# Performance work log

Measured on AMD Instinct MI355X. Metric: run time of the kernel, lower is better.

The kernel has to match this reference:

```python
import jax, jax.numpy as jnp
import numpy as np

B, F_IN, D_IN = 1024, 64, 64
N_CAPS, D_CAPS = 32, 64
ROUTINGS = 3
HEADS = 2
EPS = 1e-7  # K.epsilon()


def setup_inputs() -> dict:
    key = jax.random.key(0)
    ks = jax.random.split(key, 8)
    P = N_CAPS * (N_CAPS - 1) // 2
    return {
        "x": jax.random.normal(ks[0], (B, F_IN, D_IN), jnp.float32),
        "reweight_W": jax.random.normal(ks[1], (D_IN, N_CAPS, D_CAPS), jnp.float32) * 0.05,
        "routing_init": 10.0 * jax.random.truncated_normal(ks[2], -2.0, 2.0, (N_CAPS, F_IN), jnp.float32),
        "kernel_fm": jnp.full((N_CAPS, 1), 0.5, jnp.float32),
        "bias_fm": jnp.zeros((D_CAPS,), jnp.float32),
        "kernel_mf": jnp.ones((P, 1), jnp.float32),
        "bias_mf": jnp.zeros((D_CAPS,), jnp.float32),
        "kernel_highint": jnp.full((N_CAPS, 1), 0.5, jnp.float32),
        "bias_highint": jnp.zeros((D_CAPS * HEADS,), jnp.float32),
        "W_query": jax.random.normal(ks[3], (D_CAPS, D_CAPS * HEADS), jnp.float32) * 0.05,
        "W_key": jax.random.normal(ks[4], (D_CAPS, D_CAPS * HEADS), jnp.float32) * 0.05,
        "W_value": jax.random.normal(ks[5], (D_CAPS, D_CAPS * HEADS), jnp.float32) * 0.05,
        "W_res": jax.random.normal(ks[6], (D_CAPS, D_CAPS * HEADS), jnp.float32) * 0.05,
    }


def _squash(v):
    s = jnp.sum(v * v, axis=-1, keepdims=True) + EPS
    return (jnp.sqrt(s) / (0.5 + s)) * v


def _heads(t):
    # [B,N,H*F] -> [H,B,N,F] (matches tf.stack(tf.split(t, H, axis=2)))
    b, n, _ = t.shape
    return t.reshape(b, n, HEADS, D_CAPS).transpose(2, 0, 1, 3)


def reference(x, reweight_W, routing_init, kernel_fm, bias_fm, kernel_mf, bias_mf,
              kernel_highint, bias_highint, W_query, W_key, W_value, W_res):
    # inputs_hat: [B, N, F, C]
    inputs_hat = jnp.einsum('bfd,dnc->bnfc', x, reweight_W)
    b_logits = jnp.broadcast_to(routing_init[None], (x.shape[0], N_CAPS, F_IN))
    for _ in range(ROUTINGS):
        c = jax.nn.softmax(b_logits, axis=1)            # softmax over capsules
        outputs = _squash(jnp.einsum('bnf,bnfc->bnc', c, inputs_hat))
        b_logits = b_logits + jnp.einsum('bnc,bnfc->bnf', outputs, inputs_hat)
    c = jax.nn.softmax(b_logits, axis=1)
    routing_score = c[..., None]                        # [B,N,F,1]
    attention_output = routing_score * inputs_hat       # [B,N,F,C]

    # FM per-field: square-of-sum minus sum-of-square over input capsules
    sum_f = jnp.sum(attention_output, axis=2)           # [B,N,C]
    field_fm = sum_f ** 2 - jnp.sum(attention_output ** 2, axis=2)
    hi_fm = jnp.sum(field_fm * kernel_fm[None], axis=1) + bias_fm  # [B,C]

    field_wise_vectors = sum_f                          # [B,N,C]

    # pairwise MF interactions (itertools.combinations order == triu indices)
    li, ri = np.triu_indices(N_CAPS, k=1)
    emb_prod = field_wise_vectors[:, li] * field_wise_vectors[:, ri]  # [B,P,C]
    h_mf = jnp.sum(emb_prod * kernel_mf[None], axis=1) + bias_mf      # [B,C]

    # InteractingLayer (multi-head self-attention over fields, use_res=True)
    q = _heads(jnp.einsum('bnd,de->bne', field_wise_vectors, W_query))  # [H,B,N,F]
    k = _heads(jnp.einsum('bnd,de->bne', field_wise_vectors, W_key))
    v = _heads(jnp.einsum('bnd,de->bne', field_wise_vectors, W_value))
    attn = jax.nn.softmax(jnp.einsum('hbnf,hbmf->hbnm', q, k), axis=-1)
    out = jnp.einsum('hbnm,hbmf->hbnf', attn, v)        # [H,B,N,F]
    out = out.transpose(1, 2, 0, 3).reshape(x.shape[0], N_CAPS, HEADS * D_CAPS)
    res = jnp.einsum('bnd,de->bne', field_wise_vectors, W_res)
    fv2 = jax.nn.relu(out + res)                        # [B,N,H*F]
    high_int = jnp.sum(fv2 * kernel_highint[None], axis=1) + bias_highint  # [B,2C]

    return jnp.concatenate([hi_fm, h_mf, high_int], axis=-1), routing_score
```

## Files before the change

### kernel.cpp

```cpp
#include <hip/hip_runtime.h>


#define EPS_SQ 1e-7f

typedef __attribute__((ext_vector_type(8))) short bf16x8;
typedef __attribute__((ext_vector_type(4))) float floatx4;

__device__ __forceinline__ int lidx(int r, int c) {
  return r * 68 + ((((c >> 2) ^ (r >> 2)) & 15) << 2) + (c & 3);
}
__device__ __forceinline__ unsigned short f2bf(float f) {
  unsigned u = __float_as_uint(f);
  u += 0x7FFFu + ((u >> 16) & 1u);
  return (unsigned short)(u >> 16);
}

__global__ __launch_bounds__(256) void k_upd(
    const float* __restrict__ x, const float* __restrict__ rinit,
    const float* __restrict__ ow, float* __restrict__ blog,
    float* __restrict__ xc, float* __restrict__ rs, int iter)
{
  __shared__ __align__(16) float xs[64 * 68];
  __shared__ __align__(16) float owS[32 * 68];
  __shared__ __align__(16) float bS[32 * 68];
  const int b = blockIdx.x, t = threadIdx.x;
  const float* xb = x + b * 4096;

#pragma unroll
  for (int k = 0; k < 4; k++) {
    int lin = t + 256 * k; int f = lin >> 4; int d0 = (lin & 15) << 2;
    *(float4*)&xs[lidx(f, d0)] = *(const float4*)(xb + f * 64 + d0);
  }
  {
    const float* src = (iter <= 1) ? rinit : (blog + b * 2048);
#pragma unroll
    for (int k = 0; k < 2; k++) {
      int lin = t + 256 * k; int n = lin >> 4; int f0 = (lin & 15) << 2;
      *(float4*)&bS[lidx(n, f0)] = *(const float4*)(src + n * 64 + f0);
    }
  }
  if (iter > 0) {
#pragma unroll
    for (int k = 0; k < 2; k++) {
      int lin = t + 256 * k; int n = lin >> 4; int d0 = (lin & 15) << 2;
      *(float4*)&owS[lidx(n, d0)] = *(const float4*)(ow + b * 2048 + n * 64 + d0);
    }
  }
  __syncthreads();

  const int tn = t >> 4, tlo = t & 15;

  if (iter > 0) {
    const int n0 = tn * 2, f0 = tlo * 4;
    float acc[2][4] = {{0, 0, 0, 0}, {0, 0, 0, 0}};
    for (int dq = 0; dq < 64; dq += 4) {
      float o[2][4];
      *(float4*)o[0] = *(const float4*)&owS[lidx(n0, dq)];
      *(float4*)o[1] = *(const float4*)&owS[lidx(n0 + 1, dq)];
#pragma unroll
      for (int i = 0; i < 4; i++) {
        float xr[4];
        *(float4*)xr = *(const float4*)&xs[lidx(f0 + i, dq)];
#pragma unroll
        for (int k = 0; k < 4; k++) {
          acc[0][i] += o[0][k] * xr[k];
          acc[1][i] += o[1][k] * xr[k];
        }
      }
    }
#pragma unroll
    for (int j = 0; j < 2; j++) {
      float tmp[4];
      *(float4*)tmp = *(const float4*)&bS[lidx(n0 + j, f0)];
#pragma unroll
      for (int i = 0; i < 4; i++) tmp[i] += acc[j][i];
      *(float4*)&bS[lidx(n0 + j, f0)] = *(float4*)tmp;
    }
    __syncthreads();
    if (iter < 3) {
#pragma unroll
      for (int k = 0; k < 2; k++) {
        int lin = t + 256 * k; int n = lin >> 4; int f0b = (lin & 15) << 2;
        *(float4*)(blog + b * 2048 + n * 64 + f0b) = *(const float4*)&bS[lidx(n, f0b)];
      }
    }
    __syncthreads();
  }

  {
    const int n = t & 31, fg = t >> 5;
#pragma unroll
    for (int k = 0; k < 8; k++) {
      int f = fg * 8 + k;
      float v = bS[lidx(n, f)];
      float m = v;
      for (int s = 16; s > 0; s >>= 1) m = fmaxf(m, __shfl_xor(m, s, 64));
      float e = __expf(v - m);
      float sum = e;
      for (int s = 16; s > 0; s >>= 1) sum += __shfl_xor(sum, s, 64);
      bS[lidx(n, f)] = e / sum;
    }
  }
  __syncthreads();

  if (iter == 3) {
#pragma unroll
    for (int k = 0; k < 8; k++) {
      int lin = t + 256 * k; int n = lin >> 6, f = lin & 63;
      rs[b * 2048 + n * 64 + f] = bS[lidx(n, f)];
    }
  }
  {
    const int n0 = tn * 2, d0 = tlo * 4;
    float acc[2][4] = {{0, 0, 0, 0}, {0, 0, 0, 0}};
    for (int f = 0; f < 64; f++) {
      float c0v = bS[lidx(n0, f)];
      float c1v = bS[lidx(n0 + 1, f)];
      float xr[4];
      *(float4*)xr = *(const float4*)&xs[lidx(f, d0)];
#pragma unroll
      for (int i = 0; i < 4; i++) {
        acc[0][i] += c0v * xr[i];
        acc[1][i] += c1v * xr[i];
      }
    }
#pragma unroll
    for (int j = 0; j < 2; j++)
      *(float4*)(xc + b * 2048 + (n0 + j) * 64 + d0) = *(float4*)acc[j];
  }
}

__global__ __launch_bounds__(256) void k_prepq(
    const float* __restrict__ W, float* __restrict__ Qb)
{
  __shared__ __align__(16) float Mn[64 * 68];
  const int n = blockIdx.x, t = threadIdx.x;
#pragma unroll
  for (int k = 0; k < 4; k++) {
    int lin = t + 256 * k; int d = lin >> 4; int c0 = (lin & 15) << 2;
    *(float4*)&Mn[lidx(d, c0)] = *(const float4*)(W + d * 2048 + n * 64 + c0);
  }
  __syncthreads();
  const int d1 = (t >> 4) * 4, d2 = (t & 15) * 4;
  float acc[4][4] = {};
  for (int cq = 0; cq < 64; cq += 4) {
    float m1[4][4], m2[4][4];
#pragma unroll
    for (int i = 0; i < 4; i++) *(float4*)m1[i] = *(const float4*)&Mn[lidx(d1 + i, cq)];
#pragma unroll
    for (int j = 0; j < 4; j++) *(float4*)m2[j] = *(const float4*)&Mn[lidx(d2 + j, cq)];
#pragma unroll
    for (int i = 0; i < 4; i++)
#pragma unroll
      for (int j = 0; j < 4; j++) {
        float s = 0.f;
#pragma unroll
        for (int k = 0; k < 4; k++) s += m1[i][k] * m2[j][k];
        acc[i][j] += s;
      }
  }
#pragma unroll
  for (int i = 0; i < 4; i++)
    *(float4*)(Qb + n * 4096 + (d1 + i) * 64 + d2) = *(float4*)acc[i];
}

__global__ __launch_bounds__(256) void k_sowq(
    const float* __restrict__ Qb, const float* __restrict__ xc,
    float* __restrict__ ow)
{
  __shared__ __align__(16) float Qs[64 * 68];
  __shared__ __align__(16) float xcS[32 * 68];
  const int n = blockIdx.x & 31, b0 = (blockIdx.x >> 5) * 32, t = threadIdx.x;

#pragma unroll
  for (int k = 0; k < 4; k++) {
    int lin = t + 256 * k; int d1 = lin >> 4; int d2 = (lin & 15) << 2;
    *(float4*)&Qs[lidx(d1, d2)] = *(const float4*)(Qb + n * 4096 + d1 * 64 + d2);
  }
#pragma unroll
  for (int k = 0; k < 2; k++) {
    int lin = t + 256 * k; int bb = lin >> 4; int d0 = (lin & 15) << 2;
    *(float4*)&xcS[lidx(bb, d0)] = *(const float4*)(xc + (b0 + bb) * 2048 + n * 64 + d0);
  }
  __syncthreads();

  const int bb0 = (t >> 4) * 2, d4 = (t & 15) * 4;
  float y0[4] = {}, y1[4] = {};
  for (int dq = 0; dq < 64; dq += 4) {
    float x0[4], x1[4];
    *(float4*)x0 = *(const float4*)&xcS[lidx(bb0, dq)];
    *(float4*)x1 = *(const float4*)&xcS[lidx(bb0 + 1, dq)];
#pragma unroll
    for (int j = 0; j < 4; j++) {
      float qr[4];
      *(float4*)qr = *(const float4*)&Qs[lidx(dq + j, d4)];
#pragma unroll
      for (int c = 0; c < 4; c++) {
        y0[c] += x0[j] * qr[c];
        y1[c] += x1[j] * qr[c];
      }
    }
  }
  float xa[4], xb2[4];
  *(float4*)xa = *(const float4*)&xcS[lidx(bb0, d4)];
  *(float4*)xb2 = *(const float4*)&xcS[lidx(bb0 + 1, d4)];
  float s0 = 0.f, s1 = 0.f;
#pragma unroll
  for (int c = 0; c < 4; c++) { s0 += y0[c] * xa[c]; s1 += y1[c] * xb2[c]; }
#pragma unroll
  for (int sh = 1; sh <= 8; sh <<= 1) {
    s0 += __shfl_xor(s0, sh, 64);
    s1 += __shfl_xor(s1, sh, 64);
  }
  s0 += EPS_SQ; s1 += EPS_SQ;
  const float sc0 = sqrtf(s0) / (0.5f + s0);
  const float sc1 = sqrtf(s1) / (0.5f + s1);
  float o0[4], o1[4];
#pragma unroll
  for (int c = 0; c < 4; c++) { o0[c] = y0[c] * sc0; o1[c] = y1[c] * sc1; }
  *(float4*)(ow + (b0 + bb0) * 2048 + n * 64 + d4) = *(float4*)o0;
  *(float4*)(ow + (b0 + bb0 + 1) * 2048 + n * 64 + d4) = *(float4*)o1;
}

__global__ __launch_bounds__(256) void k_fwv(
    const float* __restrict__ W, const float* __restrict__ xc,
    float* __restrict__ fwv)
{
  __shared__ __align__(16) float Mn[64 * 68];
  __shared__ __align__(16) float xcS[32 * 68];
  const int n = blockIdx.x & 31, b0 = (blockIdx.x >> 5) * 32, t = threadIdx.x;

#pragma unroll
  for (int k = 0; k < 4; k++) {
    int lin = t + 256 * k; int d = lin >> 4; int c0 = (lin & 15) << 2;
    *(float4*)&Mn[lidx(d, c0)] = *(const float4*)(W + d * 2048 + n * 64 + c0);
  }
#pragma unroll
  for (int k = 0; k < 2; k++) {
    int lin = t + 256 * k; int bb = lin >> 4; int d0 = (lin & 15) << 2;
    *(float4*)&xcS[lidx(bb, d0)] = *(const float4*)(xc + (b0 + bb) * 2048 + n * 64 + d0);
  }
  __syncthreads();

  const int bb0 = (t >> 4) * 2, c4 = (t & 15) * 4;
  float acc[2][4] = {};
  for (int dq = 0; dq < 64; dq += 4) {
    float xv0[4], xv1[4];
    *(float4*)xv0 = *(const float4*)&xcS[lidx(bb0, dq)];
    *(float4*)xv1 = *(const float4*)&xcS[lidx(bb0 + 1, dq)];
#pragma unroll
    for (int j = 0; j < 4; j++) {
      float mr[4];
      *(float4*)mr = *(const float4*)&Mn[lidx(dq + j, c4)];
#pragma unroll
      for (int c = 0; c < 4; c++) {
        acc[0][c] += xv0[j] * mr[c];
        acc[1][c] += xv1[j] * mr[c];
      }
    }
  }
  *(float4*)(fwv + (b0 + bb0) * 2048 + n * 64 + c4) = *(float4*)acc[0];
  *(float4*)(fwv + (b0 + bb0 + 1) * 2048 + n * 64 + c4) = *(float4*)acc[1];
}

__global__ __launch_bounds__(256) void k_ih(
    const float* __restrict__ x, const float* __restrict__ W,
    const float* __restrict__ rs, float* __restrict__ ssq)
{
  __shared__ __align__(16) unsigned short xB[4 * 64 * 64];
  __shared__ __align__(16) unsigned short wB[2 * 64 * 64];
  __shared__ unsigned short cF2[4 * 8 * 64];
  const int n_oct = (blockIdx.x & 3) << 3, b0 = (blockIdx.x >> 2) * 4;
  const int t = threadIdx.x, w = t >> 6, lane = t & 63;

#pragma unroll
  for (int k = 0; k < 16; k++) {
    int ch = t + 256 * k;
    int bb = ch >> 10, rem = ch & 1023;
    int f = rem >> 4, fq = rem & 15;
    int dg = fq >> 1, half = fq & 1;
    float4 v = *(const float4*)(x + ((b0 + bb) * 64 + f) * 64 + fq * 4);
    unsigned p0 = f2bf(v.x) | ((unsigned)f2bf(v.y) << 16);
    unsigned p1 = f2bf(v.z) | ((unsigned)f2bf(v.w) << 16);
    *(uint2*)&xB[bb * 4096 + f * 64 + ((dg ^ (f & 7)) << 3) + half * 4] =
        make_uint2(p0, p1);
  }
#pragma unroll
  for (int nn = 0; nn < 8; nn++) {
    float v = rs[(b0 + w) * 2048 + (n_oct + nn) * 64 + lane];
    cF2[(w * 8 + nn) * 64 + lane] = f2bf(v * v);
  }
  __syncthreads();

  const int m = lane & 15, q = lane >> 4, ms = m & 7;
  bf16x8 a[4][2];
#pragma unroll
  for (int mi = 0; mi < 4; mi++) {
    const unsigned short* bp = xB + w * 4096 + (mi * 16 + m) * 64;
#pragma unroll
    for (int kk = 0; kk < 2; kk++)
      a[mi][kk] = *(const bf16x8*)&bp[((kk * 4 + q) ^ ms) << 3];
  }

  for (int np = 0; np < 4; np++) {
    const int n0 = n_oct + np * 2;
    __syncthreads();
    {
      int dd = t >> 2, cq = t & 3;
      int dg = dd >> 3, dl = dd & 7;
#pragma unroll
      for (int nn = 0; nn < 2; nn++) {
        const float* wp = W + dd * 2048 + (n0 + nn) * 64 + cq * 16;
        unsigned short* base = wB + nn * 4096;
#pragma unroll
        for (int i4 = 0; i4 < 4; i4++) {
          float4 v = *(const float4*)(wp + i4 * 4);
          float vv[4] = {v.x, v.y, v.z, v.w};
#pragma unroll
          for (int j = 0; j < 4; j++) {
            int c = cq * 16 + i4 * 4 + j;
            base[c * 64 + ((dg ^ (c & 7)) << 3) + dl] = f2bf(vv[j]);
          }
        }
      }
    }
    __syncthreads();
#pragma unroll
    for (int nn = 0; nn < 2; nn++) {
      bf16x8 bf[4][2];
#pragma unroll
      for (int ci = 0; ci < 4; ci++) {
        const unsigned short* bp = wB + nn * 4096 + (ci * 16 + m) * 64;
#pragma unroll
        for (int kk = 0; kk < 2; kk++)
          bf[ci][kk] = *(const bf16x8*)&bp[((kk * 4 + q) ^ ms) << 3];
      }
      float ps[4] = {0.f, 0.f, 0.f, 0.f};
      const unsigned short* cf = cF2 + (w * 8 + np * 2 + nn) * 64 + q * 4;
#pragma unroll
      for (int mi = 0; mi < 4; mi++) {
        float cfv[4];
#pragma unroll
        for (int r = 0; r < 4; r++)
          cfv[r] = __uint_as_float((unsigned)cf[mi * 16 + r] << 16);
#pragma unroll
        for (int ci = 0; ci < 4; ci++) {
          floatx4 c0 = {0.f, 0.f, 0.f, 0.f};
          c0 = __builtin_amdgcn_mfma_f32_16x16x32_bf16(a[mi][0], bf[ci][0], c0, 0, 0, 0);
          c0 = __builtin_amdgcn_mfma_f32_16x16x32_bf16(a[mi][1], bf[ci][1], c0, 0, 0, 0);
#pragma unroll
          for (int r = 0; r < 4; r++) { float tv = c0[r]; ps[ci] += cfv[r] * tv * tv; }
        }
      }
#pragma unroll
      for (int ci = 0; ci < 4; ci++) {
        ps[ci] += __shfl_xor(ps[ci], 16, 64);
        ps[ci] += __shfl_xor(ps[ci], 32, 64);
      }
      if (q == 0) {
#pragma unroll
        for (int ci = 0; ci < 4; ci++)
          ssq[(b0 + w) * 2048 + (n0 + nn) * 64 + ci * 16 + m] = ps[ci];
      }
    }
  }
}

__global__ __launch_bounds__(256) void k_prep(
    const float* __restrict__ Wq, const float* __restrict__ Wk,
    const float* __restrict__ kmf, float* __restrict__ Ab, float* __restrict__ Kb)
{
  const int t = threadIdx.x;
  if (blockIdx.x < 8) {
    __shared__ __align__(16) float wkS[64 * 68];
    __shared__ __align__(16) float wqS[16 * 68];
    const int h = blockIdx.x & 1, rg = blockIdx.x >> 1;
#pragma unroll
    for (int k = 0; k < 4; k++) {
      int lin = t + 256 * k; int dp = lin >> 4; int e0 = (lin & 15) << 2;
      *(float4*)&wkS[lidx(dp, e0)] = *(const float4*)(Wk + dp * 128 + h * 64 + e0);
    }
    {
      int dl = t >> 4, e0 = (t & 15) << 2;
      *(float4*)&wqS[lidx(dl, e0)] = *(const float4*)(Wq + (rg * 16 + dl) * 128 + h * 64 + e0);
    }
    __syncthreads();
    const int dl = t >> 4, dp0 = (t & 15) << 2;
    float acc[4] = {};
    for (int e = 0; e < 64; e += 4) {
      float q4[4];
      *(float4*)q4 = *(const float4*)&wqS[lidx(dl, e)];
#pragma unroll
      for (int c = 0; c < 4; c++) {
        float mr[4];
        *(float4*)mr = *(const float4*)&wkS[lidx(dp0 + c, e)];
        acc[c] += q4[0] * mr[0] + q4[1] * mr[1] + q4[2] * mr[2] + q4[3] * mr[3];
      }
    }
    *(float4*)(Ab + h * 4096 + (rg * 16 + dl) * 64 + dp0) = *(float4*)acc;
  } else {
    __shared__ float Ks[1024];
    *(float4*)&Ks[t * 4] = make_float4(0.f, 0.f, 0.f, 0.f);
    __syncthreads();
    if (t < 248) {
#pragma unroll
      for (int j = 0; j < 2; j++) {
        int p = t * 2 + j;
        if (p < 496) {
          int l = 0, rem = p;
          while (rem >= 31 - l) { rem -= 31 - l; ++l; }
          int r = l + 1 + rem;
          float v = kmf[p];
          Ks[l * 32 + r] = v;
          Ks[r * 32 + l] = v;
        }
      }
    }
    __syncthreads();
    *(float4*)&Kb[t * 4] = *(const float4*)&Ks[t * 4];
  }
}

__global__ __launch_bounds__(256) void k_attn(
    const float* __restrict__ fwv, const float* __restrict__ ssq,
    const float* __restrict__ Ab, const float* __restrict__ Kb,
    const float* __restrict__ Wv, const float* __restrict__ Wr,
    const float* __restrict__ kfm, const float* __restrict__ bfm,
    const float* __restrict__ bmf, const float* __restrict__ khi,
    const float* __restrict__ bhi, float* __restrict__ out0)
{
  __shared__ __align__(16) float smem[8832];
  float* fwS  = smem;
  float* pS   = smem + 2176;
  float* bufA = smem + 4480;
  float* tS   = smem + 6656;
  float* vS   = smem + 4480;
  float* redH = smem + 2176;
  float* Kf   = smem + 4480;
  float* red1 = smem + 5504;

  const int b = blockIdx.x, t = threadIdx.x;
  const int tn = t >> 4, te = t & 15;
  const int n0 = tn * 2, e0 = te * 8, d0 = te * 4;

#pragma unroll
  for (int k = 0; k < 2; k++) {
    int lin = t + 256 * k; int nn = lin >> 4; int c0 = (lin & 15) << 2;
    *(float4*)&fwS[lidx(nn, c0)] = *(const float4*)(fwv + b * 2048 + nn * 64 + c0);
  }
  __syncthreads();

  for (int h = 0; h < 2; h++) {
    float tacc[2][4] = {};
    for (int half = 0; half < 2; half++) {
#pragma unroll
      for (int k = 0; k < 2; k++) {
        int lin = t + 256 * k; int d = lin >> 4; int c0 = (lin & 15) << 2;
        *(float4*)&bufA[lidx(d, c0)] =
            *(const float4*)(Ab + h * 4096 + (half * 32 + d) * 64 + c0);
      }
      __syncthreads();
      for (int dq = 0; dq < 32; dq += 4) {
        float fw0[4], fw1[4];
        *(float4*)fw0 = *(const float4*)&fwS[lidx(n0, half * 32 + dq)];
        *(float4*)fw1 = *(const float4*)&fwS[lidx(n0 + 1, half * 32 + dq)];
#pragma unroll
        for (int j = 0; j < 4; j++) {
          float mr[4];
          *(float4*)mr = *(const float4*)&bufA[lidx(dq + j, d0)];
#pragma unroll
          for (int c = 0; c < 4; c++) {
            tacc[0][c] += fw0[j] * mr[c];
            tacc[1][c] += fw1[j] * mr[c];
          }
        }
      }
      __syncthreads();
    }
    *(float4*)&tS[lidx(n0, d0)] = *(float4*)tacc[0];
    *(float4*)&tS[lidx(n0 + 1, d0)] = *(float4*)tacc[1];
    __syncthreads();
    {
      const int m0 = te * 2;
      float s00 = 0.f, s01 = 0.f, s10 = 0.f, s11 = 0.f;
      for (int kk = 0; kk < 16; kk++) {
        float ta0[4], ta1[4], f0[4], f1[4];
        *(float4*)ta0 = *(const float4*)&tS[lidx(n0, kk * 4)];
        *(float4*)ta1 = *(const float4*)&tS[lidx(n0 + 1, kk * 4)];
        *(float4*)f0 = *(const float4*)&fwS[lidx(m0, kk * 4)];
        *(float4*)f1 = *(const float4*)&fwS[lidx(m0 + 1, kk * 4)];
#pragma unroll
        for (int j = 0; j < 4; j++) {
          s00 += ta0[j] * f0[j]; s01 += ta0[j] * f1[j];
          s10 += ta1[j] * f0[j]; s11 += ta1[j] * f1[j];
        }
      }
      pS[(h * 32 + n0) * 36 + m0] = s00;
      pS[(h * 32 + n0) * 36 + m0 + 1] = s01;
      pS[(h * 32 + n0 + 1) * 36 + m0] = s10;
      pS[(h * 32 + n0 + 1) * 36 + m0 + 1] = s11;
    }
    __syncthreads();
  }

  {
    const int r = t >> 2, sub = t & 3;
    const int base = r * 36 + sub * 8;
    float v0[4], v1[4];
    *(float4*)v0 = *(const float4*)&pS[base];
    *(float4*)v1 = *(const float4*)&pS[base + 4];
    float mx = fmaxf(fmaxf(fmaxf(v0[0], v0[1]), fmaxf(v0[2], v0[3])),
                     fmaxf(fmaxf(v1[0], v1[1]), fmaxf(v1[2], v1[3])));
    mx = fmaxf(mx, __shfl_xor(mx, 1, 64));
    mx = fmaxf(mx, __shfl_xor(mx, 2, 64));
    float sum = 0.f;
#pragma unroll
    for (int j = 0; j < 4; j++) { v0[j] = __expf(v0[j] - mx); sum += v0[j]; }
#pragma unroll
    for (int j = 0; j < 4; j++) { v1[j] = __expf(v1[j] - mx); sum += v1[j]; }
    sum += __shfl_xor(sum, 1, 64);
    sum += __shfl_xor(sum, 2, 64);
    const float inv = 1.0f / sum;
#pragma unroll
    for (int j = 0; j < 4; j++) { v0[j] *= inv; v1[j] *= inv; }
    *(float4*)&pS[base] = *(float4*)v0;
    *(float4*)&pS[base + 4] = *(float4*)v1;
  }
  __syncthreads();

  {
    float acc[2][8] = {};
    for (int dq = 0; dq < 64; dq += 4) {
      float fw0[4], fw1[4];
      *(float4*)fw0 = *(const float4*)&fwS[lidx(n0, dq)];
      *(float4*)fw1 = *(const float4*)&fwS[lidx(n0 + 1, dq)];
#pragma unroll
      for (int jj = 0; jj < 4; jj++) {
        float w8[8];
        *(float4*)&w8[0] = *(const float4*)(Wv + (dq + jj) * 128 + e0);
        *(float4*)&w8[4] = *(const float4*)(Wv + (dq + jj) * 128 + e0 + 4);
#pragma unroll
        for (int j = 0; j < 8; j++) {
          acc[0][j] += fw0[jj] * w8[j];
          acc[1][j] += fw1[jj] * w8[j];
        }
      }
    }
    *(float4*)&vS[n0 * 132 + e0] = *(float4*)&acc[0][0];
    *(float4*)&vS[n0 * 132 + e0 + 4] = *(float4*)&acc[0][4];
    *(float4*)&vS[(n0 + 1) * 132 + e0] = *(float4*)&acc[1][0];
    *(float4*)&vS[(n0 + 1) * 132 + e0 + 4] = *(float4*)&acc[1][4];
  }
  __syncthreads();

  {
    const int h2 = te >> 3;
    float pacc[2][8] = {};
    for (int m = 0; m < 32; m++) {
      float p0 = pS[(h2 * 32 + n0) * 36 + m];
      float p1 = pS[(h2 * 32 + n0 + 1) * 36 + m];
      float vr[8];
      *(float4*)&vr[0] = *(const float4*)&vS[m * 132 + e0];
      *(float4*)&vr[4] = *(const float4*)&vS[m * 132 + e0 + 4];
#pragma unroll
      for (int j = 0; j < 8; j++) {
        pacc[0][j] += p0 * vr[j];
        pacc[1][j] += p1 * vr[j];
      }
    }
    for (int dq = 0; dq < 64; dq += 4) {
      float fw0[4], fw1[4];
      *(float4*)fw0 = *(const float4*)&fwS[lidx(n0, dq)];
      *(float4*)fw1 = *(const float4*)&fwS[lidx(n0 + 1, dq)];
#pragma unroll
      for (int jj = 0; jj < 4; jj++) {
        float w8[8];
        *(float4*)&w8[0] = *(const float4*)(Wr + (dq + jj) * 128 + e0);
        *(float4*)&w8[4] = *(const float4*)(Wr + (dq + jj) * 128 + e0 + 4);
#pragma unroll
        for (int j = 0; j < 8; j++) {
          pacc[0][j] += fw0[jj] * w8[j];
          pacc[1][j] += fw1[jj] * w8[j];
        }
      }
    }
    __syncthreads();
    {
      float kh0 = khi[n0], kh1 = khi[n0 + 1];
      float ph[8];
#pragma unroll
      for (int j = 0; j < 8; j++)
        ph[j] = kh0 * fmaxf(pacc[0][j], 0.f) + kh1 * fmaxf(pacc[1][j], 0.f);
      *(float4*)&redH[tn * 132 + e0] = *(float4*)&ph[0];
      *(float4*)&redH[tn * 132 + e0 + 4] = *(float4*)&ph[4];
    }
  }
  *(float4*)&Kf[t * 4] = *(const float4*)(Kb + t * 4);
  __syncthreads();

  if (t < 128) {
    float s = 0.f;
#pragma unroll
    for (int k = 0; k < 16; k++) s += redH[k * 132 + t];
    out0[b * 256 + 128 + t] = s + bhi[t];
  }
  {
    const int c = t & 63, nq = t >> 6;
    float p = 0.f;
#pragma unroll
    for (int k = 0; k < 8; k++) {
      int nn = nq * 8 + k;
      float fv = fwS[lidx(nn, c)];
      float sv = ssq[b * 2048 + nn * 64 + c];
      p += (fv * fv - sv) * kfm[nn];
    }
    red1[nq * 68 + c] = p;
    float inner[8] = {};
    for (int r = 0; r < 32; r++) {
      float fr = fwS[lidx(r, c)];
#pragma unroll
      for (int l8 = 0; l8 < 8; l8++)
        inner[l8] += Kf[(nq * 8 + l8) * 32 + r] * fr;
    }
    float hmf = 0.f;
#pragma unroll
    for (int l8 = 0; l8 < 8; l8++)
      hmf += fwS[lidx(nq * 8 + l8, c)] * inner[l8];
    red1[(4 + nq) * 68 + c] = hmf;
  }
  __syncthreads();
  if (t < 64) {
    out0[b * 256 + t] = red1[t] + red1[68 + t] + red1[136 + t] + red1[204 + t] + bfm[t];
    float h2 = red1[272 + t] + red1[340 + t] + red1[408 + t] + red1[476 + t];
    out0[b * 256 + 64 + t] = 0.5f * h2 + bmf[t];
  }
}

extern "C" void kernel_launch(void* const* d_in, const int* in_sizes, int n_in,
                              void* d_out, int out_size, void* d_ws, size_t ws_size,
                              hipStream_t stream) {
  (void)in_sizes; (void)n_in; (void)out_size; (void)ws_size;
  const float* x     = (const float*)d_in[0];
  const float* W     = (const float*)d_in[1];
  const float* rinit = (const float*)d_in[2];
  const float* kfm   = (const float*)d_in[3];
  const float* bfm   = (const float*)d_in[4];
  const float* kmf   = (const float*)d_in[5];
  const float* bmf   = (const float*)d_in[6];
  const float* khi   = (const float*)d_in[7];
  const float* bhi   = (const float*)d_in[8];
  const float* Wq    = (const float*)d_in[9];
  const float* Wk    = (const float*)d_in[10];
  const float* Wv    = (const float*)d_in[11];
  const float* Wr    = (const float*)d_in[12];

  float* out0 = (float*)d_out;
  float* rs   = out0 + 1024 * 256;
  float* Qbuf = rs;

  float* ws   = (float*)d_ws;
  float* xc   = ws;
  float* ow   = ws + 2097152;
  float* blog = ws + 2 * 2097152;
  float* fwv  = ow;
  float* ssq  = blog;
  float* Abuf = xc;
  float* Kbuf = xc + 8192;

  k_prepq<<<32, 256, 0, stream>>>(W, Qbuf);
  k_upd<<<1024, 256, 0, stream>>>(x, rinit, ow, blog, xc, rs, 0);
  for (int it = 1; it <= 3; it++) {
    k_sowq<<<1024, 256, 0, stream>>>(Qbuf, xc, ow);
    k_upd<<<1024, 256, 0, stream>>>(x, rinit, ow, blog, xc, rs, it);
  }
  k_fwv<<<1024, 256, 0, stream>>>(W, xc, fwv);
  k_prep<<<9, 256, 0, stream>>>(Wq, Wk, kmf, Abuf, Kbuf);
  k_ih<<<1024, 256, 0, stream>>>(x, W, rs, ssq);
  k_attn<<<1024, 256, 0, stream>>>(fwv, ssq, Abuf, Kbuf, Wv, Wr,
                                   kfm, bfm, bmf, khi, bhi, out0);
}
```

Measured before the change: 280.5 us.

## Fuse all routing iterations and field-wise projection into one per-batch kernel

Replaces the alternating k_upd/k_sowq launches (seven kernels) and k_fwv with a single k_route2 kernel. Each block keeps one batch's logits, coupling coefficients, xc and outputs in shared memory across all routing iterations. The Q-matrix and W reads now come straight from global memory (via cache) instead of being staged per block. The three prep kernels merge into one 41-block launch. This removes launch overhead and the global round-trips of xc, ow and blog, at the cost of more shared memory per block and uncoalesced-ish per-thread reads of Q and W.

```diff
diff --git a/kernel.cpp b/kernel.cpp
--- a/kernel.cpp
+++ b/kernel.cpp
@@ -15,252 +15,236 @@
   return (unsigned short)(u >> 16);
 }
 
-__global__ __launch_bounds__(256) void k_upd(
-    const float* __restrict__ x, const float* __restrict__ rinit,
-    const float* __restrict__ ow, float* __restrict__ blog,
-    float* __restrict__ xc, float* __restrict__ rs, int iter)
+__global__ __launch_bounds__(256) void k_prep2(
+    const float* __restrict__ W, const float* __restrict__ Wq,
+    const float* __restrict__ Wk, const float* __restrict__ kmf,
+    float* __restrict__ Qb, float* __restrict__ Ab, float* __restrict__ Kb)
+{
+  const int t = threadIdx.x;
+  if (blockIdx.x < 32) {
+    __shared__ __align__(16) float Mn[64 * 68];
+    const int n = blockIdx.x;
+#pragma unroll
+    for (int k = 0; k < 4; k++) {
+      int lin = t + 256 * k; int d = lin >> 4; int c0 = (lin & 15) << 2;
+      *(float4*)&Mn[lidx(d, c0)] = *(const float4*)(W + d * 2048 + n * 64 + c0);
+    }
+    __syncthreads();
+    const int d1 = (t >> 4) * 4, d2 = (t & 15) * 4;
+    float acc[4][4] = {};
+    for (int cq = 0; cq < 64; cq += 4) {
+      float m1[4][4], m2[4][4];
+#pragma unroll
+      for (int i = 0; i < 4; i++) *(float4*)m1[i] = *(const float4*)&Mn[lidx(d1 + i, cq)];
+#pragma unroll
+      for (int j = 0; j < 4; j++) *(float4*)m2[j] = *(const float4*)&Mn[lidx(d2 + j, cq)];
+#pragma unroll
+      for (int i = 0; i < 4; i++)
+#pragma unroll
+        for (int j = 0; j < 4; j++) {
+          float s = 0.f;
+#pragma unroll
+          for (int k = 0; k < 4; k++) s += m1[i][k] * m2[j][k];
+          acc[i][j] += s;
+        }
+    }
+#pragma unroll
+    for (int i = 0; i < 4; i++)
+      *(float4*)(Qb + n * 4096 + (d1 + i) * 64 + d2) = *(float4*)acc[i];
+  } else if (blockIdx.x < 40) {
+    __shared__ __align__(16) float wkS[64 * 68];
+    __shared__ __align__(16) float wqS[16 * 68];
+    const int hb = blockIdx.x - 32;
+    const int h = hb & 1, rg = hb >> 1;
+#pragma unroll
+    for (int k = 0; k < 4; k++) {
+      int lin = t + 256 * k; int dp = lin >> 4; int e0 = (lin & 15) << 2;
+      *(float4*)&wkS[lidx(dp, e0)] = *(const float4*)(Wk + dp * 128 + h * 64 + e0);
+    }
+    {
+      int dl = t >> 4, e0 = (t & 15) << 2;
+      *(float4*)&wqS[lidx(dl, e0)] = *(const float4*)(Wq + (rg * 16 + dl) * 128 + h * 64 + e0);
+    }
+    __syncthreads();
+    const int dl = t >> 4, dp0 = (t & 15) << 2;
+    float acc[4] = {};
+    for (int e = 0; e < 64; e += 4) {
+      float q4[4];
+      *(float4*)q4 = *(const float4*)&wqS[lidx(dl, e)];
+#pragma unroll
+      for (int c = 0; c < 4; c++) {
+        float mr[4];
+        *(float4*)mr = *(const float4*)&wkS[lidx(dp0 + c, e)];
+        acc[c] += q4[0] * mr[0] + q4[1] * mr[1] + q4[2] * mr[2] + q4[3] * mr[3];
+      }
+    }
+    *(float4*)(Ab + h * 4096 + (rg * 16 + dl) * 64 + dp0) = *(float4*)acc;
+  } else {
+    __shared__ float Ks[1024];
+    *(float4*)&Ks[t * 4] = make_float4(0.f, 0.f, 0.f, 0.f);
+    __syncthreads();
+    if (t < 248) {
+#pragma unroll
+      for (int j = 0; j < 2; j++) {
+        int p = t * 2 + j;
+        if (p < 496) {
+          int l = 0, rem = p;
+          while (rem >= 31 - l) { rem -= 31 - l; ++l; }
+          int r = l + 1 + rem;
+          float v = kmf[p];
+          Ks[l * 32 + r] = v;
+          Ks[r * 32 + l] = v;
+        }
+      }
+    }
+    __syncthreads();
+    *(float4*)&Kb[t * 4] = *(const float4*)&Ks[t * 4];
+  }
+}
+
+__global__ __launch_bounds__(256) void k_route2(
+    const float* __restrict__ x, const float* __restrict__ W,
+    const float* __restrict__ rinit, const float* __restrict__ Qb,
+    float* __restrict__ rs, float* __restrict__ fwv)
 {
   __shared__ __align__(16) float xs[64 * 68];
+  __shared__ __align__(16) float bS[32 * 68];
+  __shared__ __align__(16) float cS[32 * 68];
+  __shared__ __align__(16) float xcS[32 * 68];
   __shared__ __align__(16) float owS[32 * 68];
-  __shared__ __align__(16) float bS[32 * 68];
   const int b = blockIdx.x, t = threadIdx.x;
-  const float* xb = x + b * 4096;
+  const int tn = t >> 4, tlo = t & 15;
+  const int nq = t >> 3, sub = t & 7;
 
 #pragma unroll
   for (int k = 0; k < 4; k++) {
     int lin = t + 256 * k; int f = lin >> 4; int d0 = (lin & 15) << 2;
-    *(float4*)&xs[lidx(f, d0)] = *(const float4*)(xb + f * 64 + d0);
-  }
+    *(float4*)&xs[lidx(f, d0)] = *(const float4*)(x + b * 4096 + f * 64 + d0);
+  }
+#pragma unroll
+  for (int k = 0; k < 2; k++) {
+    int lin = t + 256 * k; int n = lin >> 4; int f0 = (lin & 15) << 2;
+    *(float4*)&bS[lidx(n, f0)] = *(const float4*)(rinit + n * 64 + f0);
+  }
+  __syncthreads();
+
+  for (int it = 0; it < 4; it++) {
+    {
+      const int nl = t & 31, fg = t >> 5;
+#pragma unroll
+      for (int k = 0; k < 8; k++) {
+        int f = fg * 8 + k;
+        float v = bS[lidx(nl, f)];
+        float m = v;
+        for (int s = 16; s > 0; s >>= 1) m = fmaxf(m, __shfl_xor(m, s, 64));
+        float e = __expf(v - m);
+        float sum = e;
+        for (int s = 16; s > 0; s >>= 1) sum += __shfl_xor(sum, s, 64);
+        cS[lidx(nl, f)] = e / sum;
+      }
+    }
+    __syncthreads();
+    if (it == 3) {
+#pragma unroll
+      for (int k = 0; k < 8; k++) {
+        int lin = t + 256 * k; int n = lin >> 6, f = lin & 63;
+        rs[b * 2048 + n * 64 + f] = cS[lidx(n, f)];
+      }
+    }
+    {
+      const int n0 = tn * 2, d0 = tlo * 4;
+      float acc[2][4] = {{0, 0, 0, 0}, {0, 0, 0, 0}};
+      for (int f = 0; f < 64; f++) {
+        float c0v = cS[lidx(n0, f)];
+        float c1v = cS[lidx(n0 + 1, f)];
+        float xr[4];
+        *(float4*)xr = *(const float4*)&xs[lidx(f, d0)];
+#pragma unroll
+        for (int i = 0; i < 4; i++) {
+          acc[0][i] += c0v * xr[i];
+          acc[1][i] += c1v * xr[i];
+        }
+      }
+      *(float4*)&xcS[lidx(n0, d0)] = *(float4*)acc[0];
+      *(float4*)&xcS[lidx(n0 + 1, d0)] = *(float4*)acc[1];
+    }
+    __syncthreads();
+    if (it == 3) break;
+
+    {
+      const float* Qn = Qb + nq * 4096 + sub * 8;
+      float y[8] = {};
+#pragma unroll 4
+      for (int d1 = 0; d1 < 64; d1++) {
+        float xv = xcS[lidx(nq, d1)];
+        float4 qa = *(const float4*)(Qn + d1 * 64);
+        float4 qb2 = *(const float4*)(Qn + d1 * 64 + 4);
+        y[0] += xv * qa.x; y[1] += xv * qa.y; y[2] += xv * qa.z; y[3] += xv * qa.w;
+        y[4] += xv * qb2.x; y[5] += xv * qb2.y; y[6] += xv * qb2.z; y[7] += xv * qb2.w;
+      }
+      float xa[4], xb2[4];
+      *(float4*)xa = *(const float4*)&xcS[lidx(nq, sub * 8)];
+      *(float4*)xb2 = *(const float4*)&xcS[lidx(nq, sub * 8 + 4)];
+      float ps = y[0] * xa[0] + y[1] * xa[1] + y[2] * xa[2] + y[3] * xa[3]
+               + y[4] * xb2[0] + y[5] * xb2[1] + y[6] * xb2[2] + y[7] * xb2[3];
+      ps += __shfl_xor(ps, 1, 64);
+      ps += __shfl_xor(ps, 2, 64);
+      ps += __shfl_xor(ps, 4, 64);
+      const float ss = ps + EPS_SQ;
+      const float sc = sqrtf(ss) / (0.5f + ss);
+      float o0[4] = {y[0] * sc, y[1] * sc, y[2] * sc, y[3] * sc};
+      float o1[4] = {y[4] * sc, y[5] * sc, y[6] * sc, y[7] * sc};
+      *(float4*)&owS[lidx(nq, sub * 8)] = *(float4*)o0;
+      *(float4*)&owS[lidx(nq, sub * 8 + 4)] = *(float4*)o1;
+    }
+    __syncthreads();
+
+    {
+      const int n0 = tn * 2, f0 = tlo * 4;
+      float acc[2][4] = {{0, 0, 0, 0}, {0, 0, 0, 0}};
+      for (int dq = 0; dq < 64; dq += 4) {
+        float o[2][4];
+        *(float4*)o[0] = *(const float4*)&owS[lidx(n0, dq)];
+        *(float4*)o[1] = *(const float4*)&owS[lidx(n0 + 1, dq)];
+#pragma unroll
+        for (int i = 0; i < 4; i++) {
+          float xr[4];
+          *(float4*)xr = *(const float4*)&xs[lidx(f0 + i, dq)];
+#pragma unroll
+          for (int k = 0; k < 4; k++) {
+            acc[0][i] += o[0][k] * xr[k];
+            acc[1][i] += o[1][k] * xr[k];
+          }
+        }
+      }
+#pragma unroll
+      for (int j = 0; j < 2; j++) {
+        float tmp[4];
+        *(float4*)tmp = *(const float4*)&bS[lidx(n0 + j, f0)];
+#pragma unroll
+        for (int i = 0; i < 4; i++) tmp[i] += acc[j][i];
+        *(float4*)&bS[lidx(n0 + j, f0)] = *(float4*)tmp;
+      }
+    }
+    __syncthreads();
+  }
+
   {
-    const float* src = (iter <= 1) ? rinit : (blog + b * 2048);
-#pragma unroll
-    for (int k = 0; k < 2; k++) {
-      int lin = t + 256 * k; int n = lin >> 4; int f0 = (lin & 15) << 2;
-      *(float4*)&bS[lidx(n, f0)] = *(const float4*)(src + n * 64 + f0);
-    }
-  }
-  if (iter > 0) {
-#pragma unroll
-    for (int k = 0; k < 2; k++) {
-      int lin = t + 256 * k; int n = lin >> 4; int d0 = (lin & 15) << 2;
-      *(float4*)&owS[lidx(n, d0)] = *(const float4*)(ow + b * 2048 + n * 64 + d0);
-    }
-  }
-  __syncthreads();
-
-  const int tn = t >> 4, tlo = t & 15;
-
-  if (iter > 0) {
-    const int n0 = tn * 2, f0 = tlo * 4;
-    float acc[2][4] = {{0, 0, 0, 0}, {0, 0, 0, 0}};
-    for (int dq = 0; dq < 64; dq += 4) {
-      float o[2][4];
-      *(float4*)o[0] = *(const float4*)&owS[lidx(n0, dq)];
-      *(float4*)o[1] = *(const float4*)&owS[lidx(n0 + 1, dq)];
-#pragma unroll
-      for (int i = 0; i < 4; i++) {
-        float xr[4];
-        *(float4*)xr = *(const float4*)&xs[lidx(f0 + i, dq)];
-#pragma unroll
-        for (int k = 0; k < 4; k++) {
-          acc[0][i] += o[0][k] * xr[k];
-          acc[1][i] += o[1][k] * xr[k];
-        }
-      }
-    }
-#pragma unroll
-    for (int j = 0; j < 2; j++) {
-      float tmp[4];
-      *(float4*)tmp = *(const float4*)&bS[lidx(n0 + j, f0)];
-#pragma unroll
-      for (int i = 0; i < 4; i++) tmp[i] += acc[j][i];
-      *(float4*)&bS[lidx(n0 + j, f0)] = *(float4*)tmp;
-    }
-    __syncthreads();
-    if (iter < 3) {
-#pragma unroll
-      for (int k = 0; k < 2; k++) {
-        int lin = t + 256 * k; int n = lin >> 4; int f0b = (lin & 15) << 2;
-        *(float4*)(blog + b * 2048 + n * 64 + f0b) = *(const float4*)&bS[lidx(n, f0b)];
-      }
-    }
-    __syncthreads();
-  }
-
-  {
-    const int n = t & 31, fg = t >> 5;
-#pragma unroll
-    for (int k = 0; k < 8; k++) {
-      int f = fg * 8 + k;
-      float v = bS[lidx(n, f)];
-      float m = v;
-      for (int s = 16; s > 0; s >>= 1) m = fmaxf(m, __shfl_xor(m, s, 64));
-      float e = __expf(v - m);
-      float sum = e;
-      for (int s = 16; s > 0; s >>= 1) sum += __shfl_xor(sum, s, 64);
-      bS[lidx(n, f)] = e / sum;
-    }
-  }
-  __syncthreads();
-
-  if (iter == 3) {
-#pragma unroll
-    for (int k = 0; k < 8; k++) {
-      int lin = t + 256 * k; int n = lin >> 6, f = lin & 63;
-      rs[b * 2048 + n * 64 + f] = bS[lidx(n, f)];
-    }
-  }
-  {
-    const int n0 = tn * 2, d0 = tlo * 4;
-    float acc[2][4] = {{0, 0, 0, 0}, {0, 0, 0, 0}};
-    for (int f = 0; f < 64; f++) {
-      float c0v = bS[lidx(n0, f)];
-      float c1v = bS[lidx(n0 + 1, f)];
-      float xr[4];
-      *(float4*)xr = *(const float4*)&xs[lidx(f, d0)];
-#pragma unroll
-      for (int i = 0; i < 4; i++) {
-        acc[0][i] += c0v * xr[i];
-        acc[1][i] += c1v * xr[i];
-      }
-    }
-#pragma unroll
-    for (int j = 0; j < 2; j++)
-      *(float4*)(xc + b * 2048 + (n0 + j) * 64 + d0) = *(float4*)acc[j];
-  }
-}
-
-__global__ __launch_bounds__(256) void k_prepq(
-    const float* __restrict__ W, float* __restrict__ Qb)
-{
-  __shared__ __align__(16) float Mn[64 * 68];
-  const int n = blockIdx.x, t = threadIdx.x;
-#pragma unroll
-  for (int k = 0; k < 4; k++) {
-    int lin = t + 256 * k; int d = lin >> 4; int c0 = (lin & 15) << 2;
-    *(float4*)&Mn[lidx(d, c0)] = *(const float4*)(W + d * 2048 + n * 64 + c0);
-  }
-  __syncthreads();
-  const int d1 = (t >> 4) * 4, d2 = (t & 15) * 4;
-  float acc[4][4] = {};
-  for (int cq = 0; cq < 64; cq += 4) {
-    float m1[4][4], m2[4][4];
-#pragma unroll
-    for (int i = 0; i < 4; i++) *(float4*)m1[i] = *(const float4*)&Mn[lidx(d1 + i, cq)];
-#pragma unroll
-    for (int j = 0; j < 4; j++) *(float4*)m2[j] = *(const float4*)&Mn[lidx(d2 + j, cq)];
-#pragma unroll
-    for (int i = 0; i < 4; i++)
-#pragma unroll
-      for (int j = 0; j < 4; j++) {
-        float s = 0.f;
-#pragma unroll
-        for (int k = 0; k < 4; k++) s += m1[i][k] * m2[j][k];
-        acc[i][j] += s;
-      }
-  }
-#pragma unroll
-  for (int i = 0; i < 4; i++)
-    *(float4*)(Qb + n * 4096 + (d1 + i) * 64 + d2) = *(float4*)acc[i];
-}
-
-__global__ __launch_bounds__(256) void k_sowq(
-    const float* __restrict__ Qb, const float* __restrict__ xc,
-    float* __restrict__ ow)
-{
-  __shared__ __align__(16) float Qs[64 * 68];
-  __shared__ __align__(16) float xcS[32 * 68];
-  const int n = blockIdx.x & 31, b0 = (blockIdx.x >> 5) * 32, t = threadIdx.x;
-
-#pragma unroll
-  for (int k = 0; k < 4; k++) {
-    int lin = t + 256 * k; int d1 = lin >> 4; int d2 = (lin & 15) << 2;
-    *(float4*)&Qs[lidx(d1, d2)] = *(const float4*)(Qb + n * 4096 + d1 * 64 + d2);
-  }
-#pragma unroll
-  for (int k = 0; k < 2; k++) {
-    int lin = t + 256 * k; int bb = lin >> 4; int d0 = (lin & 15) << 2;
-    *(float4*)&xcS[lidx(bb, d0)] = *(const float4*)(xc + (b0 + bb) * 2048 + n * 64 + d0);
-  }
-  __syncthreads();
-
-  const int bb0 = (t >> 4) * 2, d4 = (t & 15) * 4;
-  float y0[4] = {}, y1[4] = {};
-  for (int dq = 0; dq < 64; dq += 4) {
-    float x0[4], x1[4];
-    *(float4*)x0 = *(const float4*)&xcS[lidx(bb0, dq)];
-    *(float4*)x1 = *(const float4*)&xcS[lidx(bb0 + 1, dq)];
-#pragma unroll
-    for (int j = 0; j < 4; j++) {
-      float qr[4];
-      *(float4*)qr = *(const float4*)&Qs[lidx(dq + j, d4)];
-#pragma unroll
-      for (int c = 0; c < 4; c++) {
-        y0[c] += x0[j] * qr[c];
-        y1[c] += x1[j] * qr[c];
-      }
-    }
-  }
-  float xa[4], xb2[4];
-  *(float4*)xa = *(const float4*)&xcS[lidx(bb0, d4)];
-  *(float4*)xb2 = *(const float4*)&xcS[lidx(bb0 + 1, d4)];
-  float s0 = 0.f, s1 = 0.f;
-#pragma unroll
-  for (int c = 0; c < 4; c++) { s0 += y0[c] * xa[c]; s1 += y1[c] * xb2[c]; }
-#pragma unroll
-  for (int sh = 1; sh <= 8; sh <<= 1) {
-    s0 += __shfl_xor(s0, sh, 64);
-    s1 += __shfl_xor(s1, sh, 64);
-  }
-  s0 += EPS_SQ; s1 += EPS_SQ;
-  const float sc0 = sqrtf(s0) / (0.5f + s0);
-  const float sc1 = sqrtf(s1) / (0.5f + s1);
-  float o0[4], o1[4];
-#pragma unroll
-  for (int c = 0; c < 4; c++) { o0[c] = y0[c] * sc0; o1[c] = y1[c] * sc1; }
-  *(float4*)(ow + (b0 + bb0) * 2048 + n * 64 + d4) = *(float4*)o0;
-  *(float4*)(ow + (b0 + bb0 + 1) * 2048 + n * 64 + d4) = *(float4*)o1;
-}
-
-__global__ __launch_bounds__(256) void k_fwv(
-    const float* __restrict__ W, const float* __restrict__ xc,
-    float* __restrict__ fwv)
-{
-  __shared__ __align__(16) float Mn[64 * 68];
-  __shared__ __align__(16) float xcS[32 * 68];
-  const int n = blockIdx.x & 31, b0 = (blockIdx.x >> 5) * 32, t = threadIdx.x;
-
-#pragma unroll
-  for (int k = 0; k < 4; k++) {
-    int lin = t + 256 * k; int d = lin >> 4; int c0 = (lin & 15) << 2;
-    *(float4*)&Mn[lidx(d, c0)] = *(const float4*)(W + d * 2048 + n * 64 + c0);
-  }
-#pragma unroll
-  for (int k = 0; k < 2; k++) {
-    int lin = t + 256 * k; int bb = lin >> 4; int d0 = (lin & 15) << 2;
-    *(float4*)&xcS[lidx(bb, d0)] = *(const float4*)(xc + (b0 + bb) * 2048 + n * 64 + d0);
-  }
-  __syncthreads();
-
-  const int bb0 = (t >> 4) * 2, c4 = (t & 15) * 4;
-  float acc[2][4] = {};
-  for (int dq = 0; dq < 64; dq += 4) {
-    float xv0[4], xv1[4];
-    *(float4*)xv0 = *(const float4*)&xcS[lidx(bb0, dq)];
-    *(float4*)xv1 = *(const float4*)&xcS[lidx(bb0 + 1, dq)];
-#pragma unroll
-    for (int j = 0; j < 4; j++) {
-      float mr[4];
-      *(float4*)mr = *(const float4*)&Mn[lidx(dq + j, c4)];
-#pragma unroll
-      for (int c = 0; c < 4; c++) {
-        acc[0][c] += xv0[j] * mr[c];
-        acc[1][c] += xv1[j] * mr[c];
-      }
-    }
-  }
-  *(float4*)(fwv + (b0 + bb0) * 2048 + n * 64 + c4) = *(float4*)acc[0];
-  *(float4*)(fwv + (b0 + bb0 + 1) * 2048 + n * 64 + c4) = *(float4*)acc[1];
+    const float* Wn = W + nq * 64 + sub * 8;
+    float a8[8] = {};
+#pragma unroll 4
+    for (int d = 0; d < 64; d++) {
+      float xv = xcS[lidx(nq, d)];
+      float4 wa = *(const float4*)(Wn + d * 2048);
+      float4 wb = *(const float4*)(Wn + d * 2048 + 4);
+      a8[0] += xv * wa.x; a8[1] += xv * wa.y; a8[2] += xv * wa.z; a8[3] += xv * wa.w;
+      a8[4] += xv * wb.x; a8[5] += xv * wb.y; a8[6] += xv * wb.z; a8[7] += xv * wb.w;
+    }
+    float o0[4] = {a8[0], a8[1], a8[2], a8[3]};
+    float o1[4] = {a8[4], a8[5], a8[6], a8[7]};
+    *(float4*)(fwv + b * 2048 + nq * 64 + sub * 8) = *(float4*)o0;
+    *(float4*)(fwv + b * 2048 + nq * 64 + sub * 8 + 4) = *(float4*)o1;
+  }
 }
 
 __global__ __launch_bounds__(256) void k_ih(
@@ -363,61 +347,6 @@
           ssq[(b0 + w) * 2048 + (n0 + nn) * 64 + ci * 16 + m] = ps[ci];
       }
     }
-  }
-}
-
-__global__ __launch_bounds__(256) void k_prep(
-    const float* __restrict__ Wq, const float* __restrict__ Wk,
-    const float* __restrict__ kmf, float* __restrict__ Ab, float* __restrict__ Kb)
-{
-  const int t = threadIdx.x;
-  if (blockIdx.x < 8) {
-    __shared__ __align__(16) float wkS[64 * 68];
-    __shared__ __align__(16) float wqS[16 * 68];
-    const int h = blockIdx.x & 1, rg = blockIdx.x >> 1;
-#pragma unroll
-    for (int k = 0; k < 4; k++) {
-      int lin = t + 256 * k; int dp = lin >> 4; int e0 = (lin & 15) << 2;
-      *(float4*)&wkS[lidx(dp, e0)] = *(const float4*)(Wk + dp * 128 + h * 64 + e0);
-    }
-    {
-      int dl = t >> 4, e0 = (t & 15) << 2;
-      *(float4*)&wqS[lidx(dl, e0)] = *(const float4*)(Wq + (rg * 16 + dl) * 128 + h * 64 + e0);
-    }
-    __syncthreads();
-    const int dl = t >> 4, dp0 = (t & 15) << 2;
-    float acc[4] = {};
-    for (int e = 0; e < 64; e += 4) {
-      float q4[4];
-      *(float4*)q4 = *(const float4*)&wqS[lidx(dl, e)];
-#pragma unroll
-      for (int c = 0; c < 4; c++) {
-        float mr[4];
-        *(float4*)mr = *(const float4*)&wkS[lidx(dp0 + c, e)];
-        acc[c] += q4[0] * mr[0] + q4[1] * mr[1] + q4[2] * mr[2] + q4[3] * mr[3];
-      }
-    }
-    *(float4*)(Ab + h * 4096 + (rg * 16 + dl) * 64 + dp0) = *(float4*)acc;
-  } else {
-    __shared__ float Ks[1024];
-    *(float4*)&Ks[t * 4] = make_float4(0.f, 0.f, 0.f, 0.f);
-    __syncthreads();
-    if (t < 248) {
-#pragma unroll
-      for (int j = 0; j < 2; j++) {
-        int p = t * 2 + j;
-        if (p < 496) {
-          int l = 0, rem = p;
-          while (rem >= 31 - l) { rem -= 31 - l; ++l; }
-          int r = l + 1 + rem;
-          float v = kmf[p];
-          Ks[l * 32 + r] = v;
-          Ks[r * 32 + l] = v;
-        }
-      }
-    }
-    __syncthreads();
-    *(float4*)&Kb[t * 4] = *(const float4*)&Ks[t * 4];
   }
 }
 
@@ -656,25 +585,16 @@
 
   float* out0 = (float*)d_out;
   float* rs   = out0 + 1024 * 256;
-  float* Qbuf = rs;
 
   float* ws   = (float*)d_ws;
-  float* xc   = ws;
-  float* ow   = ws + 2097152;
-  float* blog = ws + 2 * 2097152;
-  float* fwv  = ow;
-  float* ssq  = blog;
-  float* Abuf = xc;
-  float* Kbuf = xc + 8192;
-
-  k_prepq<<<32, 256, 0, stream>>>(W, Qbuf);
-  k_upd<<<1024, 256, 0, stream>>>(x, rinit, ow, blog, xc, rs, 0);
-  for (int it = 1; it <= 3; it++) {
-    k_sowq<<<1024, 256, 0, stream>>>(Qbuf, xc, ow);
-    k_upd<<<1024, 256, 0, stream>>>(x, rinit, ow, blog, xc, rs, it);
-  }
-  k_fwv<<<1024, 256, 0, stream>>>(W, xc, fwv);
-  k_prep<<<9, 256, 0, stream>>>(Wq, Wk, kmf, Abuf, Kbuf);
+  float* Abuf = ws;
+  float* Kbuf = ws + 8192;
+  float* Qbuf = ws + 16384;
+  float* fwv  = ws + 2097152;
+  float* ssq  = ws + 2 * 2097152;
+
+  k_prep2<<<41, 256, 0, stream>>>(W, Wq, Wk, kmf, Qbuf, Abuf, Kbuf);
+  k_route2<<<1024, 256, 0, stream>>>(x, W, rinit, Qbuf, rs, fwv);
   k_ih<<<1024, 256, 0, stream>>>(x, W, rs, ssq);
   k_attn<<<1024, 256, 0, stream>>>(fwv, ssq, Abuf, Kbuf, Wv, Wr,
                                    kfm, bfm, bmf, khi, bhi, out0);
```

Result: no change. 279.6 us (-0.3%).
